# Kernel optimization log

Hardware: AMD Instinct MI355X
Metric: run time of the kernel (lower is better)

The kernel has to match this reference:

```python
import jax, jax.numpy as jnp
import numpy as np

D_IN = 2048
D_OUT = 2048
N_HEADS = 32
N_KV = 8
HEAD_DIM = D_OUT // N_HEADS  # 64
CTX = 2048
ROPE_BASE = 10000.0


def _rope_tables(head_dim, ctx, base):
    inv_freq = 1.0 / base ** (np.arange(0, head_dim, 2, dtype=np.float32) / head_dim)
    pos = np.arange(ctx, dtype=np.float32)
    ang = pos[:, None] * inv_freq[None, :]          # [ctx, hd/2]
    ang = np.concatenate([ang, ang], axis=1)         # [ctx, hd]
    return jnp.asarray(np.cos(ang)), jnp.asarray(np.sin(ang))


def _apply_rope(x, cos, sin):
    # x: [b, h, n, hd]; cos/sin: [n, hd]
    half = x.shape[-1] // 2
    x1, x2 = x[..., :half], x[..., half:]
    rotated = jnp.concatenate([-x2, x1], axis=-1)
    return x * cos + rotated * sin


def setup_inputs() -> dict:
    key = jax.random.key(0)
    ks = jax.random.split(key, 5)
    b, n = 1, 2048
    x = jax.random.normal(ks[0], (b, n, D_IN), dtype=jnp.float32)
    s = 0.02
    Wq = jax.random.normal(ks[1], (D_IN, D_OUT), dtype=jnp.float32) * s
    Wk = jax.random.normal(ks[2], (D_IN, N_KV * HEAD_DIM), dtype=jnp.float32) * s
    Wv = jax.random.normal(ks[3], (D_IN, N_KV * HEAD_DIM), dtype=jnp.float32) * s
    Wo = jax.random.normal(ks[4], (D_OUT, D_OUT), dtype=jnp.float32) * s
    cos, sin = _rope_tables(HEAD_DIM, CTX, ROPE_BASE)
    return {"x": x, "Wq": Wq, "Wk": Wk, "Wv": Wv, "Wo": Wo, "cos": cos, "sin": sin}


def reference(x, Wq, Wk, Wv, Wo, cos, sin):
    b, n, _ = x.shape
    gs = N_HEADS // N_KV  # group size
    q = (x @ Wq).reshape(b, n, N_HEADS, HEAD_DIM).transpose(0, 2, 1, 3)  # [b,H,n,d]
    k = (x @ Wk).reshape(b, n, N_KV, HEAD_DIM).transpose(0, 2, 1, 3)     # [b,G,n,d]
    v = (x @ Wv).reshape(b, n, N_KV, HEAD_DIM).transpose(0, 2, 1, 3)
    q = _apply_rope(q, cos[:n], sin[:n])
    k = _apply_rope(k, cos[:n], sin[:n])
    # GQA: view queries as [b, G, gs, n, d]; broadcast K/V over the group axis
    qg = q.reshape(b, N_KV, gs, n, HEAD_DIM)
    scores = jnp.einsum('bgrnd,bgmd->bgrnm', qg, k) / HEAD_DIM ** 0.5
    causal = jnp.triu(jnp.ones((n, n), dtype=bool), k=1)
    scores = jnp.where(causal, -jnp.inf, scores)
    w = jax.nn.softmax(scores, axis=-1)
    ctx = jnp.einsum('bgrnm,bgmd->bgrnd', w, v)           # [b,G,gs,n,d]
    ctx = ctx.reshape(b, N_HEADS, n, HEAD_DIM).transpose(0, 2, 1, 3).reshape(b, n, D_OUT)
    return ctx @ Wo
```

## Files before the change

### kernel.cpp

```cpp
#include <hip/hip_runtime.h>
#include <hip/hip_bf16.h>

typedef __bf16 bf16x8 __attribute__((ext_vector_type(8)));
typedef float f32x4 __attribute__((ext_vector_type(4)));
typedef unsigned u32x4 __attribute__((ext_vector_type(4)));

#define MFMA16 __builtin_amdgcn_mfma_f32_16x16x32_bf16

#define GLD16(gp, lp) __builtin_amdgcn_global_load_lds( \
    (const __attribute__((address_space(1))) void*)(gp), \
    (__attribute__((address_space(3))) void*)(lp), 16, 0, 0)

__device__ __forceinline__ unsigned short f2bf(float f) {
  __hip_bfloat16 h = __float2bfloat16(f);
  return *(unsigned short*)&h;
}

__global__ __launch_bounds__(256)
void convert_bf16_kernel(const float* __restrict__ in, unsigned short* __restrict__ out) {
  int i = blockIdx.x * 256 + threadIdx.x;
  float4 a = *(const float4*)&in[i * 8];
  float4 b = *(const float4*)&in[i * 8 + 4];
  uint4 o;
  o.x = (unsigned)f2bf(a.x) | ((unsigned)f2bf(a.y) << 16);
  o.y = (unsigned)f2bf(a.z) | ((unsigned)f2bf(a.w) << 16);
  o.z = (unsigned)f2bf(b.x) | ((unsigned)f2bf(b.y) << 16);
  o.w = (unsigned)f2bf(b.z) | ((unsigned)f2bf(b.w) << 16);
  *(uint4*)&out[i * 8] = o;
}

__global__ __launch_bounds__(256)
void transpose_bf16_kernel(const float* __restrict__ in, unsigned short* __restrict__ out,
                           int K, int N) {
  __shared__ float tile[64][68];
  const int t = threadIdx.x;
  const int k0 = blockIdx.y * 64, n0 = blockIdx.x * 64;
#pragma unroll
  for (int i = 0; i < 4; ++i) {
    int r = i * 16 + (t >> 4);
    int cc = (t & 15) * 4;
    float4 v = *(const float4*)&in[(k0 + r) * N + n0 + cc];
    tile[r][cc] = v.x; tile[r][cc + 1] = v.y; tile[r][cc + 2] = v.z; tile[r][cc + 3] = v.w;
  }
  __syncthreads();
#pragma unroll
  for (int i = 0; i < 2; ++i) {
    int on = i * 32 + (t >> 3);
    int ok = (t & 7) * 8;
    uint4 o;
    o.x = (unsigned)f2bf(tile[ok + 0][on]) | ((unsigned)f2bf(tile[ok + 1][on]) << 16);
    o.y = (unsigned)f2bf(tile[ok + 2][on]) | ((unsigned)f2bf(tile[ok + 3][on]) << 16);
    o.z = (unsigned)f2bf(tile[ok + 4][on]) | ((unsigned)f2bf(tile[ok + 5][on]) << 16);
    o.w = (unsigned)f2bf(tile[ok + 6][on]) | ((unsigned)f2bf(tile[ok + 7][on]) << 16);
    *(uint4*)&out[(n0 + on) * K + k0 + ok] = o;
  }
}

__global__ __launch_bounds__(256)
void qkv_gemm_kernel(const unsigned short* __restrict__ xb,
                     const unsigned short* __restrict__ Wqt,
                     const unsigned short* __restrict__ Wkt,
                     const unsigned short* __restrict__ Wvt,
                     const float* __restrict__ cosT, const float* __restrict__ sinT,
                     unsigned short* __restrict__ Qb, unsigned short* __restrict__ Kb,
                     unsigned short* __restrict__ Vt)
{
  __shared__ unsigned short Al[2][64 * 64];
  __shared__ unsigned short Bl[2][128 * 64];
  const int t = threadIdx.x;
  const int w = t >> 6, l = t & 63, g = l >> 4, c = l & 15;
  const int wr = w >> 1, wc = w & 1;
  const int r0 = blockIdx.y * 64;
  const int c0 = blockIdx.x * 128;

  const unsigned short* B; int brow0;
  if (c0 < 2048)      { B = Wqt; brow0 = c0; }
  else if (c0 < 2560) { B = Wkt; brow0 = c0 - 2048; }
  else                { B = Wvt; brow0 = c0 - 2560; }

  f32x4 acc[2][4];
#pragma unroll
  for (int m = 0; m < 2; ++m)
#pragma unroll
    for (int n = 0; n < 4; ++n) acc[m][n] = (f32x4){0.f, 0.f, 0.f, 0.f};

  const int srow = t >> 3;
  const int scol = ((t & 7) ^ (srow & 7)) * 8;
  const unsigned dbase = (unsigned)(w * 512);

#define QKV_STAGE(buf, kt_) do {                                              \
    GLD16(&xb[(r0 + srow) * 2048 + (kt_) + scol],        &Al[buf][dbase]);    \
    GLD16(&xb[(r0 + 32 + srow) * 2048 + (kt_) + scol],   &Al[buf][2048 + dbase]); \
    GLD16(&B[(brow0 + srow) * 2048 + (kt_) + scol],      &Bl[buf][dbase]);    \
    GLD16(&B[(brow0 + 32 + srow) * 2048 + (kt_) + scol], &Bl[buf][2048 + dbase]); \
    GLD16(&B[(brow0 + 64 + srow) * 2048 + (kt_) + scol], &Bl[buf][4096 + dbase]); \
    GLD16(&B[(brow0 + 96 + srow) * 2048 + (kt_) + scol], &Bl[buf][6144 + dbase]); \
  } while (0)

  QKV_STAGE(0, 0);
  __syncthreads();

  int cur = 0;
  for (int kt = 0; kt < 2048; kt += 64) {
    if (kt + 64 < 2048) QKV_STAGE(cur ^ 1, kt + 64);
#pragma unroll
    for (int ks = 0; ks < 2; ++ks) {
      const int slot = ((ks * 4 + g) ^ (c & 7)) * 8;
      bf16x8 aF[2], bF[4];
#pragma unroll
      for (int m = 0; m < 2; ++m)
        aF[m] = *(const bf16x8*)&Al[cur][(wr * 32 + m * 16 + c) * 64 + slot];
#pragma unroll
      for (int n = 0; n < 4; ++n)
        bF[n] = *(const bf16x8*)&Bl[cur][(wc * 64 + n * 16 + c) * 64 + slot];
#pragma unroll
      for (int m = 0; m < 2; ++m)
#pragma unroll
        for (int n = 0; n < 4; ++n)
          acc[m][n] = MFMA16(aF[m], bF[n], acc[m][n], 0, 0, 0);
    }
    __syncthreads();
    cur ^= 1;
  }
#undef QKV_STAGE

  const int wcol0 = c0 + wc * 64;
  if (c0 < 2560) {
    unsigned short* dst; int hh;
    if (c0 < 2048) { dst = Qb; hh = wcol0 >> 6; }
    else           { dst = Kb; hh = (wcol0 - 2048) >> 6; }
#pragma unroll
    for (int m = 0; m < 2; ++m) {
#pragma unroll
      for (int j = 0; j < 4; ++j) {
        int p = r0 + wr * 32 + m * 16 + g * 4 + j;
#pragma unroll
        for (int n = 0; n < 2; ++n) {
          int d = n * 16 + c;
          float cv = cosT[p * 64 + d];
          float sv = sinT[p * 64 + d];
          float lo = acc[m][n][j], hi = acc[m][n + 2][j];
          dst[(hh * 2048 + p) * 64 + d]      = f2bf(lo * cv - hi * sv);
          dst[(hh * 2048 + p) * 64 + d + 32] = f2bf(hi * cv + lo * sv);
        }
      }
    }
  } else {
    int kvh = (wcol0 - 2560) >> 6;
#pragma unroll
    for (int m = 0; m < 2; ++m) {
      int p0 = r0 + wr * 32 + m * 16 + g * 4;
      int ps = (p0 & ~0x1C) | ((p0 & 0x0C) << 1) | ((p0 & 0x10) >> 2);
#pragma unroll
      for (int n = 0; n < 4; ++n) {
        int d = n * 16 + c;
        ushort4 u;
        u.x = f2bf(acc[m][n][0]); u.y = f2bf(acc[m][n][1]);
        u.z = f2bf(acc[m][n][2]); u.w = f2bf(acc[m][n][3]);
        *(ushort4*)&Vt[(kvh * 64 + d) * 2048 + ps] = u;
      }
    }
  }
}

__global__ __launch_bounds__(256)
void attn_kernel(const unsigned short* __restrict__ Qb,
                 const unsigned short* __restrict__ Kb,
                 const unsigned short* __restrict__ Vt,
                 unsigned short* __restrict__ ctxO)
{
  __shared__ unsigned short Kl[2][64 * 64];
  __shared__ unsigned short Vl[2][64 * 64];
  const int t = threadIdx.x, w = t >> 6, l = t & 63, g = l >> 4, c = l & 15;

  const int B = blockIdx.x;
  const int h = B & 31;
  const int qt = (B < 256) ? (15 - (B >> 5)) : ((B - 256) >> 5);
  const int kvh = h >> 2;
  const int qb0 = qt * 128;
  const int qb = qb0 + w * 32;

  const float C1 = 0.18033688f;
  const float MB = 23.0831067f;

  const int sr1 = t >> 3;
  const int sr2 = sr1 + 32;
  const int sc1 = ((t & 7) ^ (sr1 & 7)) * 8;
  const int sc2 = ((t & 7) ^ (sr2 & 7)) * 8;
  const unsigned ld1 = (unsigned)t * 8;
  const unsigned ld2 = ld1 + 2048;

  const unsigned short* Kh = Kb + kvh * 2048 * 64;
  const unsigned short* Vh = Vt + kvh * 64 * 2048;

  bf16x8 qf[2][2];
#pragma unroll
  for (int m = 0; m < 2; ++m)
#pragma unroll
    for (int ks = 0; ks < 2; ++ks)
      qf[m][ks] = *(const bf16x8*)&Qb[(h * 2048 + qb + m * 16 + c) * 64 + ks * 32 + g * 8];

  f32x4 ctx[2][4];
  float lsum[2] = {0.f, 0.f};
#pragma unroll
  for (int m = 0; m < 2; ++m)
#pragma unroll
    for (int n = 0; n < 4; ++n) ctx[m][n] = (f32x4){0.f, 0.f, 0.f, 0.f};

  const int NT = qb0 / 64 + 2;
  const int myNT = (qb + 32 + 63) >> 6;

  GLD16(&Kh[(0 + sr1) * 64 + sc1], &Kl[0][ld1]);
  GLD16(&Kh[(0 + sr2) * 64 + sc2], &Kl[0][ld2]);
  GLD16(&Vh[sr1 * 2048 + 0 + sc1], &Vl[0][ld1]);
  GLD16(&Vh[sr2 * 2048 + 0 + sc2], &Vl[0][ld2]);
  __syncthreads();

  int cur = 0;
  for (int ti = 0; ti < NT; ++ti) {
    if (ti + 1 < NT) {
      const int nb = (ti + 1) * 64;
      GLD16(&Kh[(nb + sr1) * 64 + sc1], &Kl[cur ^ 1][ld1]);
      GLD16(&Kh[(nb + sr2) * 64 + sc2], &Kl[cur ^ 1][ld2]);
      GLD16(&Vh[sr1 * 2048 + nb + sc1], &Vl[cur ^ 1][ld1]);
      GLD16(&Vh[sr2 * 2048 + nb + sc2], &Vl[cur ^ 1][ld2]);
    }

    if (ti < myNT) {
      const int kvb = ti * 64;

      f32x4 ST[4][2];
#pragma unroll
      for (int nn = 0; nn < 4; ++nn)
#pragma unroll
        for (int m = 0; m < 2; ++m) ST[nn][m] = (f32x4){0.f, 0.f, 0.f, 0.f};

#pragma unroll
      for (int ks = 0; ks < 2; ++ks) {
        bf16x8 kF[4];
#pragma unroll
        for (int nn = 0; nn < 4; ++nn) {
          int slot = (ks * 4 + g) ^ (c & 7);
          kF[nn] = *(const bf16x8*)&Kl[cur][(nn * 16 + c) * 64 + slot * 8];
        }
#pragma unroll
        for (int nn = 0; nn < 4; ++nn)
#pragma unroll
          for (int m = 0; m < 2; ++m)
            ST[nn][m] = MFMA16(kF[nn], qf[m][ks], ST[nn][m], 0, 0, 0);
      }

      if (kvb + 63 > qb) {
#pragma unroll
        for (int nn = 0; nn < 4; ++nn)
#pragma unroll
          for (int j = 0; j < 4; ++j) {
            int kpos = kvb + nn * 16 + g * 4 + j;
#pragma unroll
            for (int m = 0; m < 2; ++m) {
              int qpos = qb + m * 16 + c;
              if (kpos > qpos) ST[nn][m][j] = -1e30f;
            }
          }
      }

#pragma unroll
      for (int nn = 0; nn < 4; ++nn)
#pragma unroll
        for (int m = 0; m < 2; ++m)
#pragma unroll
          for (int j = 0; j < 4; ++j) {
            float p = exp2f(fmaf(ST[nn][m][j], C1, -MB));
            ST[nn][m][j] = p;
            lsum[m] += p;
          }

      unsigned pk[4][2][2];
#pragma unroll
      for (int nn = 0; nn < 4; ++nn)
#pragma unroll
        for (int m = 0; m < 2; ++m) {
          pk[nn][m][0] = (unsigned)f2bf(ST[nn][m][0]) | ((unsigned)f2bf(ST[nn][m][1]) << 16);
          pk[nn][m][1] = (unsigned)f2bf(ST[nn][m][2]) | ((unsigned)f2bf(ST[nn][m][3]) << 16);
        }

      bf16x8 pa[2][2];
#pragma unroll
      for (int m = 0; m < 2; ++m)
#pragma unroll
        for (int ks = 0; ks < 2; ++ks) {
          u32x4 pw;
          pw[0] = pk[2 * ks][m][0];
          pw[1] = pk[2 * ks][m][1];
          pw[2] = pk[2 * ks + 1][m][0];
          pw[3] = pk[2 * ks + 1][m][1];
          union { u32x4 u; bf16x8 b; } cvt; cvt.u = pw;
          pa[m][ks] = cvt.b;
        }

#pragma unroll
      for (int ks = 0; ks < 2; ++ks) {
        bf16x8 vF[4];
#pragma unroll
        for (int n = 0; n < 4; ++n) {
          int slot = (ks * 4 + g) ^ (c & 7);
          vF[n] = *(const bf16x8*)&Vl[cur][(n * 16 + c) * 64 + slot * 8];
        }
#pragma unroll
        for (int m = 0; m < 2; ++m)
#pragma unroll
          for (int n = 0; n < 4; ++n)
            ctx[m][n] = MFMA16(pa[m][ks], vF[n], ctx[m][n], 0, 0, 0);
      }
    }

    __syncthreads();
    cur ^= 1;
  }

  float inv[2];
#pragma unroll
  for (int m = 0; m < 2; ++m) {
    float rs = lsum[m];
    rs += __shfl_xor(rs, 16);
    rs += __shfl_xor(rs, 32);
    inv[m] = 1.f / rs;
  }
  float invj[2][4];
#pragma unroll
  for (int m = 0; m < 2; ++m)
#pragma unroll
    for (int j = 0; j < 4; ++j)
      invj[m][j] = __shfl(inv[m], (l & 48) + g * 4 + j);

#pragma unroll
  for (int m = 0; m < 2; ++m)
#pragma unroll
    for (int n = 0; n < 4; ++n)
#pragma unroll
      for (int j = 0; j < 4; ++j) {
        int p = qb + m * 16 + g * 4 + j;
        int d = n * 16 + c;
        ctxO[p * 2048 + h * 64 + d] = f2bf(ctx[m][n][j] * invj[m][j]);
      }
}

__global__ __launch_bounds__(256)
void out_gemm_kernel(const unsigned short* __restrict__ ctxB,
                     const unsigned short* __restrict__ Wot,
                     float* __restrict__ out)
{
  __shared__ unsigned short Al[2][64 * 64];
  __shared__ unsigned short Bl[2][128 * 64];
  const int t = threadIdx.x;
  const int w = t >> 6, l = t & 63, g = l >> 4, c = l & 15;
  const int wr = w >> 1, wc = w & 1;
  const int r0 = blockIdx.y * 64;
  const int c0 = blockIdx.x * 128;

  f32x4 acc[2][4];
#pragma unroll
  for (int m = 0; m < 2; ++m)
#pragma unroll
    for (int n = 0; n < 4; ++n) acc[m][n] = (f32x4){0.f, 0.f, 0.f, 0.f};

  const int srow = t >> 3;
  const int scol = ((t & 7) ^ (srow & 7)) * 8;
  const unsigned dbase = (unsigned)(w * 512);

#define OUT_STAGE(buf, kt_) do {                                               \
    GLD16(&ctxB[(r0 + srow) * 2048 + (kt_) + scol],      &Al[buf][dbase]);     \
    GLD16(&ctxB[(r0 + 32 + srow) * 2048 + (kt_) + scol], &Al[buf][2048 + dbase]); \
    GLD16(&Wot[(c0 + srow) * 2048 + (kt_) + scol],       &Bl[buf][dbase]);     \
    GLD16(&Wot[(c0 + 32 + srow) * 2048 + (kt_) + scol],  &Bl[buf][2048 + dbase]); \
    GLD16(&Wot[(c0 + 64 + srow) * 2048 + (kt_) + scol],  &Bl[buf][4096 + dbase]); \
    GLD16(&Wot[(c0 + 96 + srow) * 2048 + (kt_) + scol],  &Bl[buf][6144 + dbase]); \
  } while (0)

  OUT_STAGE(0, 0);
  __syncthreads();

  int cur = 0;
  for (int kt = 0; kt < 2048; kt += 64) {
    if (kt + 64 < 2048) OUT_STAGE(cur ^ 1, kt + 64);
#pragma unroll
    for (int ks = 0; ks < 2; ++ks) {
      const int slot = ((ks * 4 + g) ^ (c & 7)) * 8;
      bf16x8 aF[2], bF[4];
#pragma unroll
      for (int m = 0; m < 2; ++m)
        aF[m] = *(const bf16x8*)&Al[cur][(wr * 32 + m * 16 + c) * 64 + slot];
#pragma unroll
      for (int n = 0; n < 4; ++n)
        bF[n] = *(const bf16x8*)&Bl[cur][(wc * 64 + n * 16 + c) * 64 + slot];
#pragma unroll
      for (int m = 0; m < 2; ++m)
#pragma unroll
        for (int n = 0; n < 4; ++n)
          acc[m][n] = MFMA16(aF[m], bF[n], acc[m][n], 0, 0, 0);
    }
    __syncthreads();
    cur ^= 1;
  }
#undef OUT_STAGE

#pragma unroll
  for (int m = 0; m < 2; ++m)
#pragma unroll
    for (int j = 0; j < 4; ++j) {
      int p = r0 + wr * 32 + m * 16 + g * 4 + j;
#pragma unroll
      for (int n = 0; n < 4; ++n)
        out[p * 2048 + c0 + wc * 64 + n * 16 + c] = acc[m][n][j];
    }
}

extern "C" void kernel_launch(void* const* d_in, const int* in_sizes, int n_in,
                              void* d_out, int out_size, void* d_ws, size_t ws_size,
                              hipStream_t stream) {
  const float* x    = (const float*)d_in[0];
  const float* Wq   = (const float*)d_in[1];
  const float* Wk   = (const float*)d_in[2];
  const float* Wv   = (const float*)d_in[3];
  const float* Wo   = (const float*)d_in[4];
  const float* cosT = (const float*)d_in[5];
  const float* sinT = (const float*)d_in[6];
  float* out = (float*)d_out;

  unsigned short* xb   = (unsigned short*)d_ws;
  unsigned short* Wot  = xb;
  unsigned short* Wqt  = xb + 4 * 1024 * 1024;
  unsigned short* ctxB = Wqt;
  unsigned short* Wkt  = Wqt + 4 * 1024 * 1024;
  unsigned short* Wvt  = Wkt + 1024 * 1024;
  unsigned short* Qb   = Wvt + 1024 * 1024;
  unsigned short* Kb   = Qb + 4 * 1024 * 1024;
  unsigned short* Vt   = Kb + 1024 * 1024;

  convert_bf16_kernel<<<2048, 256, 0, stream>>>(x, xb);
  transpose_bf16_kernel<<<dim3(32, 32), 256, 0, stream>>>(Wq, Wqt, 2048, 2048);
  transpose_bf16_kernel<<<dim3(8, 32), 256, 0, stream>>>(Wk, Wkt, 2048, 512);
  transpose_bf16_kernel<<<dim3(8, 32), 256, 0, stream>>>(Wv, Wvt, 2048, 512);

  qkv_gemm_kernel<<<dim3(24, 32), 256, 0, stream>>>(xb, Wqt, Wkt, Wvt, cosT, sinT, Qb, Kb, Vt);

  transpose_bf16_kernel<<<dim3(32, 32), 256, 0, stream>>>(Wo, Wot, 2048, 2048);

  attn_kernel<<<512, 256, 0, stream>>>(Qb, Kb, Vt, ctxB);
  out_gemm_kernel<<<dim3(16, 32), 256, 0, stream>>>(ctxB, Wot, out);
}
```

Before: 143.2 us.

## Split attention into 64-row query tiles with 128-thread blocks and MFMA priority

```diff
diff --git a/kernel.cpp b/kernel.cpp
--- a/kernel.cpp
+++ b/kernel.cpp
@@ -163,7 +163,7 @@
   }
 }
 
-__global__ __launch_bounds__(256)
+__global__ __launch_bounds__(128)
 void attn_kernel(const unsigned short* __restrict__ Qb,
                  const unsigned short* __restrict__ Kb,
                  const unsigned short* __restrict__ Vt,
@@ -175,24 +175,33 @@
 
   const int B = blockIdx.x;
   const int h = B & 31;
-  const int qt = (B < 256) ? (15 - (B >> 5)) : ((B - 256) >> 5);
+  const int qt64 = (B < 512) ? (31 - (B >> 5)) : ((B - 512) >> 5);
   const int kvh = h >> 2;
-  const int qb0 = qt * 128;
+  const int qb0 = qt64 * 64;
   const int qb = qb0 + w * 32;
+  const int NT = qt64 + 1;
 
   const float C1 = 0.18033688f;
   const float MB = 23.0831067f;
 
-  const int sr1 = t >> 3;
-  const int sr2 = sr1 + 32;
-  const int sc1 = ((t & 7) ^ (sr1 & 7)) * 8;
-  const int sc2 = ((t & 7) ^ (sr2 & 7)) * 8;
-  const unsigned ld1 = (unsigned)t * 8;
-  const unsigned ld2 = ld1 + 2048;
+  const int srow = t >> 3;
+  const int scol = ((t & 7) ^ (srow & 7)) * 8;
+  const unsigned ldb = (unsigned)t * 8;
 
   const unsigned short* Kh = Kb + kvh * 2048 * 64;
   const unsigned short* Vh = Vt + kvh * 64 * 2048;
 
+#define ATTN_STAGE(buf, nb_) do {                                        \
+    GLD16(&Kh[((nb_) + srow) * 64 + scol],      &Kl[buf][ldb]);          \
+    GLD16(&Kh[((nb_) + 16 + srow) * 64 + scol], &Kl[buf][1024 + ldb]);   \
+    GLD16(&Kh[((nb_) + 32 + srow) * 64 + scol], &Kl[buf][2048 + ldb]);   \
+    GLD16(&Kh[((nb_) + 48 + srow) * 64 + scol], &Kl[buf][3072 + ldb]);   \
+    GLD16(&Vh[srow * 2048 + (nb_) + scol],        &Vl[buf][ldb]);        \
+    GLD16(&Vh[(16 + srow) * 2048 + (nb_) + scol], &Vl[buf][1024 + ldb]); \
+    GLD16(&Vh[(32 + srow) * 2048 + (nb_) + scol], &Vl[buf][2048 + ldb]); \
+    GLD16(&Vh[(48 + srow) * 2048 + (nb_) + scol], &Vl[buf][3072 + ldb]); \
+  } while (0)
+
   bf16x8 qf[2][2];
 #pragma unroll
   for (int m = 0; m < 2; ++m)
@@ -207,116 +216,107 @@
 #pragma unroll
     for (int n = 0; n < 4; ++n) ctx[m][n] = (f32x4){0.f, 0.f, 0.f, 0.f};
 
-  const int NT = qb0 / 64 + 2;
-  const int myNT = (qb + 32 + 63) >> 6;
-
-  GLD16(&Kh[(0 + sr1) * 64 + sc1], &Kl[0][ld1]);
-  GLD16(&Kh[(0 + sr2) * 64 + sc2], &Kl[0][ld2]);
-  GLD16(&Vh[sr1 * 2048 + 0 + sc1], &Vl[0][ld1]);
-  GLD16(&Vh[sr2 * 2048 + 0 + sc2], &Vl[0][ld2]);
+  ATTN_STAGE(0, 0);
   __syncthreads();
 
   int cur = 0;
   for (int ti = 0; ti < NT; ++ti) {
-    if (ti + 1 < NT) {
-      const int nb = (ti + 1) * 64;
-      GLD16(&Kh[(nb + sr1) * 64 + sc1], &Kl[cur ^ 1][ld1]);
-      GLD16(&Kh[(nb + sr2) * 64 + sc2], &Kl[cur ^ 1][ld2]);
-      GLD16(&Vh[sr1 * 2048 + nb + sc1], &Vl[cur ^ 1][ld1]);
-      GLD16(&Vh[sr2 * 2048 + nb + sc2], &Vl[cur ^ 1][ld2]);
-    }
-
-    if (ti < myNT) {
-      const int kvb = ti * 64;
-
-      f32x4 ST[4][2];
+    if (ti + 1 < NT) ATTN_STAGE(cur ^ 1, (ti + 1) * 64);
+
+    const int kvb = ti * 64;
+
+    f32x4 ST[4][2];
+#pragma unroll
+    for (int nn = 0; nn < 4; ++nn)
+#pragma unroll
+      for (int m = 0; m < 2; ++m) ST[nn][m] = (f32x4){0.f, 0.f, 0.f, 0.f};
+
+    __builtin_amdgcn_s_setprio(1);
+#pragma unroll
+    for (int ks = 0; ks < 2; ++ks) {
+      bf16x8 kF[4];
+#pragma unroll
+      for (int nn = 0; nn < 4; ++nn) {
+        int slot = (ks * 4 + g) ^ (c & 7);
+        kF[nn] = *(const bf16x8*)&Kl[cur][(nn * 16 + c) * 64 + slot * 8];
+      }
 #pragma unroll
       for (int nn = 0; nn < 4; ++nn)
 #pragma unroll
-        for (int m = 0; m < 2; ++m) ST[nn][m] = (f32x4){0.f, 0.f, 0.f, 0.f};
-
+        for (int m = 0; m < 2; ++m)
+          ST[nn][m] = MFMA16(kF[nn], qf[m][ks], ST[nn][m], 0, 0, 0);
+    }
+    __builtin_amdgcn_s_setprio(0);
+
+    if (kvb + 63 > qb) {
+#pragma unroll
+      for (int nn = 0; nn < 4; ++nn)
+#pragma unroll
+        for (int j = 0; j < 4; ++j) {
+          int kpos = kvb + nn * 16 + g * 4 + j;
+#pragma unroll
+          for (int m = 0; m < 2; ++m) {
+            int qpos = qb + m * 16 + c;
+            if (kpos > qpos) ST[nn][m][j] = -1e30f;
+          }
+        }
+    }
+
+#pragma unroll
+    for (int nn = 0; nn < 4; ++nn)
+#pragma unroll
+      for (int m = 0; m < 2; ++m)
+#pragma unroll
+        for (int j = 0; j < 4; ++j) {
+          float p = exp2f(fmaf(ST[nn][m][j], C1, -MB));
+          ST[nn][m][j] = p;
+          lsum[m] += p;
+        }
+
+    unsigned pk[4][2][2];
+#pragma unroll
+    for (int nn = 0; nn < 4; ++nn)
+#pragma unroll
+      for (int m = 0; m < 2; ++m) {
+        pk[nn][m][0] = (unsigned)f2bf(ST[nn][m][0]) | ((unsigned)f2bf(ST[nn][m][1]) << 16);
+        pk[nn][m][1] = (unsigned)f2bf(ST[nn][m][2]) | ((unsigned)f2bf(ST[nn][m][3]) << 16);
+      }
+
+    bf16x8 pa[2][2];
+#pragma unroll
+    for (int m = 0; m < 2; ++m)
 #pragma unroll
       for (int ks = 0; ks < 2; ++ks) {
-        bf16x8 kF[4];
-#pragma unroll
-        for (int nn = 0; nn < 4; ++nn) {
-          int slot = (ks * 4 + g) ^ (c & 7);
-          kF[nn] = *(const bf16x8*)&Kl[cur][(nn * 16 + c) * 64 + slot * 8];
-        }
-#pragma unroll
-        for (int nn = 0; nn < 4; ++nn)
-#pragma unroll
-          for (int m = 0; m < 2; ++m)
-            ST[nn][m] = MFMA16(kF[nn], qf[m][ks], ST[nn][m], 0, 0, 0);
-      }
-
-      if (kvb + 63 > qb) {
-#pragma unroll
-        for (int nn = 0; nn < 4; ++nn)
-#pragma unroll
-          for (int j = 0; j < 4; ++j) {
-            int kpos = kvb + nn * 16 + g * 4 + j;
-#pragma unroll
-            for (int m = 0; m < 2; ++m) {
-              int qpos = qb + m * 16 + c;
-              if (kpos > qpos) ST[nn][m][j] = -1e30f;
-            }
-          }
-      }
-
-#pragma unroll
-      for (int nn = 0; nn < 4; ++nn)
-#pragma unroll
-        for (int m = 0; m < 2; ++m)
-#pragma unroll
-          for (int j = 0; j < 4; ++j) {
-            float p = exp2f(fmaf(ST[nn][m][j], C1, -MB));
-            ST[nn][m][j] = p;
-            lsum[m] += p;
-          }
-
-      unsigned pk[4][2][2];
-#pragma unroll
-      for (int nn = 0; nn < 4; ++nn)
-#pragma unroll
-        for (int m = 0; m < 2; ++m) {
-          pk[nn][m][0] = (unsigned)f2bf(ST[nn][m][0]) | ((unsigned)f2bf(ST[nn][m][1]) << 16);
-          pk[nn][m][1] = (unsigned)f2bf(ST[nn][m][2]) | ((unsigned)f2bf(ST[nn][m][3]) << 16);
-        }
-
-      bf16x8 pa[2][2];
-#pragma unroll
-      for (int m = 0; m < 2; ++m)
-#pragma unroll
-        for (int ks = 0; ks < 2; ++ks) {
-          u32x4 pw;
-          pw[0] = pk[2 * ks][m][0];
-          pw[1] = pk[2 * ks][m][1];
-          pw[2] = pk[2 * ks + 1][m][0];
-          pw[3] = pk[2 * ks + 1][m][1];
-          union { u32x4 u; bf16x8 b; } cvt; cvt.u = pw;
-          pa[m][ks] = cvt.b;
-        }
-
-#pragma unroll
-      for (int ks = 0; ks < 2; ++ks) {
-        bf16x8 vF[4];
-#pragma unroll
-        for (int n = 0; n < 4; ++n) {
-          int slot = (ks * 4 + g) ^ (c & 7);
-          vF[n] = *(const bf16x8*)&Vl[cur][(n * 16 + c) * 64 + slot * 8];
-        }
-#pragma unroll
-        for (int m = 0; m < 2; ++m)
-#pragma unroll
-          for (int n = 0; n < 4; ++n)
-            ctx[m][n] = MFMA16(pa[m][ks], vF[n], ctx[m][n], 0, 0, 0);
-      }
-    }
+        u32x4 pw;
+        pw[0] = pk[2 * ks][m][0];
+        pw[1] = pk[2 * ks][m][1];
+        pw[2] = pk[2 * ks + 1][m][0];
+        pw[3] = pk[2 * ks + 1][m][1];
+        union { u32x4 u; bf16x8 b; } cvt; cvt.u = pw;
+        pa[m][ks] = cvt.b;
+      }
+
+    __builtin_amdgcn_s_setprio(1);
+#pragma unroll
+    for (int ks = 0; ks < 2; ++ks) {
+      bf16x8 vF[4];
+#pragma unroll
+      for (int n = 0; n < 4; ++n) {
+        int slot = (ks * 4 + g) ^ (c & 7);
+        vF[n] = *(const bf16x8*)&Vl[cur][(n * 16 + c) * 64 + slot * 8];
+      }
+#pragma unroll
+      for (int m = 0; m < 2; ++m)
+#pragma unroll
+        for (int n = 0; n < 4; ++n)
+          ctx[m][n] = MFMA16(pa[m][ks], vF[n], ctx[m][n], 0, 0, 0);
+    }
+    __builtin_amdgcn_s_setprio(0);
 
     __syncthreads();
     cur ^= 1;
   }
+#undef ATTN_STAGE
 
   float inv[2];
 #pragma unroll
@@ -446,6 +446,6 @@
 
   transpose_bf16_kernel<<<dim3(32, 32), 256, 0, stream>>>(Wo, Wot, 2048, 2048);
 
-  attn_kernel<<<512, 256, 0, stream>>>(Qb, Kb, Vt, ctxB);
+  attn_kernel<<<1024, 128, 0, stream>>>(Qb, Kb, Vt, ctxB);
   out_gemm_kernel<<<dim3(16, 32), 256, 0, stream>>>(ctxB, Wot, out);
 }
```

Measured after the change: 154.1 us. 7.6% more time.

## Split attention KV range across two blocks and combine partials afterward

Applied to the files above, without the earlier changes.

```diff
diff --git a/kernel.cpp b/kernel.cpp
--- a/kernel.cpp
+++ b/kernel.cpp
@@ -14,6 +14,9 @@
 __device__ __forceinline__ unsigned short f2bf(float f) {
   __hip_bfloat16 h = __float2bfloat16(f);
   return *(unsigned short*)&h;
+}
+__device__ __forceinline__ float bf2f(unsigned short u) {
+  union { unsigned u; float f; } v; v.u = ((unsigned)u) << 16; return v.f;
 }
 
 __global__ __launch_bounds__(256)
@@ -167,18 +170,23 @@
 void attn_kernel(const unsigned short* __restrict__ Qb,
                  const unsigned short* __restrict__ Kb,
                  const unsigned short* __restrict__ Vt,
-                 unsigned short* __restrict__ ctxO)
+                 unsigned short* __restrict__ pA, unsigned short* __restrict__ pB,
+                 float* __restrict__ lsA, float* __restrict__ lsB)
 {
   __shared__ unsigned short Kl[2][64 * 64];
   __shared__ unsigned short Vl[2][64 * 64];
   const int t = threadIdx.x, w = t >> 6, l = t & 63, g = l >> 4, c = l & 15;
 
-  const int B = blockIdx.x;
-  const int h = B & 31;
-  const int qt = (B < 256) ? (15 - (B >> 5)) : ((B - 256) >> 5);
+  static const int qt_order[16] = {15,14,13,12, 0,1,2,3, 11,10,9,8, 4,5,6,7};
+  const int b = blockIdx.x;
+  const int h = b & 31;
+  const int half = (b >> 5) & 1;
+  const int qt = qt_order[b >> 6];
   const int kvh = h >> 2;
-  const int qb0 = qt * 128;
-  const int qb = qb0 + w * 32;
+  const int qb = qt * 128 + w * 32;
+  const int t0 = half * (qt + 1);
+  const int t1 = t0 + (qt + 1);
+  const int myNT = (qb + 32 + 63) >> 6;
 
   const float C1 = 0.18033688f;
   const float MB = 23.0831067f;
@@ -193,6 +201,13 @@
   const unsigned short* Kh = Kb + kvh * 2048 * 64;
   const unsigned short* Vh = Vt + kvh * 64 * 2048;
 
+#define ATTN_STAGE(buf, nb_) do {                                  \
+    GLD16(&Kh[((nb_) + sr1) * 64 + sc1], &Kl[buf][ld1]);           \
+    GLD16(&Kh[((nb_) + sr2) * 64 + sc2], &Kl[buf][ld2]);           \
+    GLD16(&Vh[sr1 * 2048 + (nb_) + sc1], &Vl[buf][ld1]);           \
+    GLD16(&Vh[sr2 * 2048 + (nb_) + sc2], &Vl[buf][ld2]);           \
+  } while (0)
+
   bf16x8 qf[2][2];
 #pragma unroll
   for (int m = 0; m < 2; ++m)
@@ -207,24 +222,12 @@
 #pragma unroll
     for (int n = 0; n < 4; ++n) ctx[m][n] = (f32x4){0.f, 0.f, 0.f, 0.f};
 
-  const int NT = qb0 / 64 + 2;
-  const int myNT = (qb + 32 + 63) >> 6;
-
-  GLD16(&Kh[(0 + sr1) * 64 + sc1], &Kl[0][ld1]);
-  GLD16(&Kh[(0 + sr2) * 64 + sc2], &Kl[0][ld2]);
-  GLD16(&Vh[sr1 * 2048 + 0 + sc1], &Vl[0][ld1]);
-  GLD16(&Vh[sr2 * 2048 + 0 + sc2], &Vl[0][ld2]);
+  ATTN_STAGE(0, t0 * 64);
   __syncthreads();
 
   int cur = 0;
-  for (int ti = 0; ti < NT; ++ti) {
-    if (ti + 1 < NT) {
-      const int nb = (ti + 1) * 64;
-      GLD16(&Kh[(nb + sr1) * 64 + sc1], &Kl[cur ^ 1][ld1]);
-      GLD16(&Kh[(nb + sr2) * 64 + sc2], &Kl[cur ^ 1][ld2]);
-      GLD16(&Vh[sr1 * 2048 + nb + sc1], &Vl[cur ^ 1][ld1]);
-      GLD16(&Vh[sr2 * 2048 + nb + sc2], &Vl[cur ^ 1][ld2]);
-    }
+  for (int ti = t0; ti < t1; ++ti) {
+    if (ti + 1 < t1) ATTN_STAGE(cur ^ 1, (ti + 1) * 64);
 
     if (ti < myNT) {
       const int kvb = ti * 64;
@@ -235,6 +238,7 @@
 #pragma unroll
         for (int m = 0; m < 2; ++m) ST[nn][m] = (f32x4){0.f, 0.f, 0.f, 0.f};
 
+      __builtin_amdgcn_s_setprio(1);
 #pragma unroll
       for (int ks = 0; ks < 2; ++ks) {
         bf16x8 kF[4];
@@ -249,6 +253,7 @@
           for (int m = 0; m < 2; ++m)
             ST[nn][m] = MFMA16(kF[nn], qf[m][ks], ST[nn][m], 0, 0, 0);
       }
+      __builtin_amdgcn_s_setprio(0);
 
       if (kvb + 63 > qb) {
 #pragma unroll
@@ -298,6 +303,7 @@
           pa[m][ks] = cvt.b;
         }
 
+      __builtin_amdgcn_s_setprio(1);
 #pragma unroll
       for (int ks = 0; ks < 2; ++ks) {
         bf16x8 vF[4];
@@ -312,27 +318,24 @@
           for (int n = 0; n < 4; ++n)
             ctx[m][n] = MFMA16(pa[m][ks], vF[n], ctx[m][n], 0, 0, 0);
       }
+      __builtin_amdgcn_s_setprio(0);
     }
 
     __syncthreads();
     cur ^= 1;
   }
-
-  float inv[2];
+#undef ATTN_STAGE
+
+  unsigned short* pOut = half ? pB : pA;
+  float* lsOut = half ? lsB : lsA;
+
 #pragma unroll
   for (int m = 0; m < 2; ++m) {
     float rs = lsum[m];
     rs += __shfl_xor(rs, 16);
     rs += __shfl_xor(rs, 32);
-    inv[m] = 1.f / rs;
-  }
-  float invj[2][4];
-#pragma unroll
-  for (int m = 0; m < 2; ++m)
-#pragma unroll
-    for (int j = 0; j < 4; ++j)
-      invj[m][j] = __shfl(inv[m], (l & 48) + g * 4 + j);
-
+    if (l < 16) lsOut[h * 2048 + qb + m * 16 + l] = rs;
+  }
 #pragma unroll
   for (int m = 0; m < 2; ++m)
 #pragma unroll
@@ -341,8 +344,36 @@
       for (int j = 0; j < 4; ++j) {
         int p = qb + m * 16 + g * 4 + j;
         int d = n * 16 + c;
-        ctxO[p * 2048 + h * 64 + d] = f2bf(ctx[m][n][j] * invj[m][j]);
-      }
+        pOut[p * 2048 + h * 64 + d] = f2bf(ctx[m][n][j]);
+      }
+}
+
+__global__ __launch_bounds__(256)
+void combine_kernel(const unsigned short* __restrict__ pA,
+                    unsigned short* __restrict__ pB_out,
+                    const float* __restrict__ lsA, const float* __restrict__ lsB)
+{
+  const int idx = (blockIdx.x * 256 + threadIdx.x) * 8;
+  const int p = idx >> 11;
+  const int col = idx & 2047;
+  const int h = col >> 6;
+  const float inv = 1.f / (lsA[h * 2048 + p] + lsB[h * 2048 + p]);
+
+  ushort4 a0 = *(const ushort4*)&pA[idx];
+  ushort4 a1 = *(const ushort4*)&pA[idx + 4];
+  ushort4 b0 = *(const ushort4*)&pB_out[idx];
+  ushort4 b1 = *(const ushort4*)&pB_out[idx + 4];
+  ushort4 o0, o1;
+  o0.x = f2bf((bf2f(a0.x) + bf2f(b0.x)) * inv);
+  o0.y = f2bf((bf2f(a0.y) + bf2f(b0.y)) * inv);
+  o0.z = f2bf((bf2f(a0.z) + bf2f(b0.z)) * inv);
+  o0.w = f2bf((bf2f(a0.w) + bf2f(b0.w)) * inv);
+  o1.x = f2bf((bf2f(a1.x) + bf2f(b1.x)) * inv);
+  o1.y = f2bf((bf2f(a1.y) + bf2f(b1.y)) * inv);
+  o1.z = f2bf((bf2f(a1.z) + bf2f(b1.z)) * inv);
+  o1.w = f2bf((bf2f(a1.w) + bf2f(b1.w)) * inv);
+  *(ushort4*)&pB_out[idx]     = o0;
+  *(ushort4*)&pB_out[idx + 4] = o1;
 }
 
 __global__ __launch_bounds__(256)
@@ -428,11 +459,14 @@
   float* out = (float*)d_out;
 
   unsigned short* xb   = (unsigned short*)d_ws;
+  unsigned short* pA   = xb;
   unsigned short* Wot  = xb;
   unsigned short* Wqt  = xb + 4 * 1024 * 1024;
   unsigned short* ctxB = Wqt;
   unsigned short* Wkt  = Wqt + 4 * 1024 * 1024;
+  float*          lsA  = (float*)Wkt;
   unsigned short* Wvt  = Wkt + 1024 * 1024;
+  float*          lsB  = (float*)Wvt;
   unsigned short* Qb   = Wvt + 1024 * 1024;
   unsigned short* Kb   = Qb + 4 * 1024 * 1024;
   unsigned short* Vt   = Kb + 1024 * 1024;
@@ -444,8 +478,9 @@
 
   qkv_gemm_kernel<<<dim3(24, 32), 256, 0, stream>>>(xb, Wqt, Wkt, Wvt, cosT, sinT, Qb, Kb, Vt);
 
+  attn_kernel<<<1024, 256, 0, stream>>>(Qb, Kb, Vt, pA, ctxB, lsA, lsB);
+  combine_kernel<<<2048, 256, 0, stream>>>(pA, ctxB, lsA, lsB);
+
   transpose_bf16_kernel<<<dim3(32, 32), 256, 0, stream>>>(Wo, Wot, 2048, 2048);
-
-  attn_kernel<<<512, 256, 0, stream>>>(Qb, Kb, Vt, ctxB);
   out_gemm_kernel<<<dim3(16, 32), 256, 0, stream>>>(ctxB, Wot, out);
 }
```

Result: faster. 136.2 us (-4.8%).
